# Kernel tuning notes

Hardware: AMD Instinct MI355X
Metric: run time of the kernel (lower is better)

Reference implementation:

```python
import jax, jax.numpy as jnp
import numpy as np


def setup_inputs() -> dict:
    key = jax.random.key(0)
    kq, kk, kv = jax.random.split(key, 3)
    B, H, N, D = 2, 16, 2048, 64
    q = jax.random.normal(kq, (B, H, N, D), dtype=jnp.float32)
    k = jax.random.normal(kk, (B, H, N, D), dtype=jnp.float32)
    v = jax.random.normal(kv, (B, H, N, D), dtype=jnp.float32)
    return {"q": q, "k": k, "v": v}


def reference(q, k, v):
    # RBF-kernel causal attention: logits = -relu(||q-k||^2) / sqrt(D)
    B, H, N, D = q.shape
    sm_scale = 1.0 / jnp.sqrt(jnp.asarray(D, dtype=q.dtype))
    q_sq = jnp.sum(q * q, axis=-1)              # [B,H,N]
    k_sq = jnp.sum(k * k, axis=-1)              # [B,H,N]
    qk = jnp.einsum("bhmd,bhnd->bhmn", q, k)    # [B,H,N,N]
    dist_sq = q_sq[..., :, None] + k_sq[..., None, :] - 2.0 * qk
    dist_sq = jnp.maximum(dist_sq, 0.0)         # relu on squared distance
    logits = -dist_sq * sm_scale
    # causal mask: query m attends to keys n <= m
    causal = jnp.tril(jnp.ones((N, N), dtype=bool))
    logits = jnp.where(causal, logits, -jnp.inf)
    p = jax.nn.softmax(logits, axis=-1)
    out = jnp.einsum("bhmn,bhnd->bhmd", p, v)
    return out
```

## Files before the change

### kernel.cpp

```cpp
#include <hip/hip_runtime.h>

#define NN 2048
#define DD 64
#define C1 0.36067376f
#define C1H 0.18033688f

typedef _Float16 h8 __attribute__((ext_vector_type(8)));
typedef _Float16 h4 __attribute__((ext_vector_type(4)));
typedef float f32x16 __attribute__((ext_vector_type(16)));

union H8U4 { h8 v; unsigned u[4]; };

__global__ __launch_bounds__(64) void prep(const float* __restrict__ k,
                                           const float* __restrict__ v,
                                           _Float16* __restrict__ Ks,
                                           _Float16* __restrict__ Vs,
                                           float* __restrict__ hk) {
    __shared__ _Float16 T[32][72];
    const int jj = blockIdx.x, bh = blockIdx.y, lane = threadIdx.x;
    const int ln = lane & 31, lh = lane >> 5;
    const size_t ibase = (size_t)bh * NN * DD + (size_t)jj * 32 * DD;

    {
        const float* kr = k + ibase + (size_t)ln * DD;
        float s = 0.f;
#pragma unroll
        for (int c = 0; c < 4; ++c) {
            float4 a = *(const float4*)&kr[16 * c + 8 * lh];
            float4 b = *(const float4*)&kr[16 * c + 8 * lh + 4];
            h8 o = {(_Float16)a.x, (_Float16)a.y, (_Float16)a.z, (_Float16)a.w,
                    (_Float16)b.x, (_Float16)b.y, (_Float16)b.z, (_Float16)b.w};
            *(h8*)&Ks[((size_t)bh * 16384 + jj * 256 + c * 64 + lh * 32 + ln) * 8] = o;
            s += a.x*a.x + a.y*a.y + a.z*a.z + a.w*a.w
               + b.x*b.x + b.y*b.y + b.z*b.z + b.w*b.w;
        }
        s += __shfl_xor(s, 32);
        if (lh == 0) hk[bh * NN + jj * 32 + ln] = s * C1H;
    }

#pragma unroll
    for (int t = 0; t < 8; ++t) {
        int f = lane + 64 * t;
        int row = f >> 4, c4 = (f & 15) * 4;
        float4 a = *(const float4*)&v[ibase + (size_t)row * DD + c4];
        h4 hv = {(_Float16)a.x, (_Float16)a.y, (_Float16)a.z, (_Float16)a.w};
        *(h4*)&T[row][c4] = hv;
    }
    __syncthreads();
#pragma unroll
    for (int oc = 0; oc < 4; ++oc) {
        int o = oc >> 1, c = oc & 1;
        h8 r;
#pragma unroll
        for (int jx = 0; jx < 8; ++jx) r[jx] = T[16 * c + 8 * lh + jx][32 * o + ln];
        *(h8*)&Vs[((size_t)bh * 16384 + jj * 256 + o * 128 + c * 64 + lh * 32 + ln) * 8] = r;
    }
}

__global__ __launch_bounds__(128, 2) void rbf_attn(
    const float* __restrict__ q, const _Float16* __restrict__ Ks,
    const _Float16* __restrict__ Vs, const float* __restrict__ hk,
    float* __restrict__ out)
{
    __shared__ float sm[64][34];
    const int tid = threadIdx.x;
    const int bh = blockIdx.x;
    const int qt = 63 - (int)blockIdx.y;
    const int wv = tid >> 6, lane = tid & 63;
    const int ln = lane & 31, lh = lane >> 5;
    const int qrow = qt * 32 + ln;
    const size_t fbase = (size_t)bh * NN * DD;

    h8 qf[4];
    {
        const float* qr = q + fbase + (size_t)qrow * DD;
#pragma unroll
        for (int c = 0; c < 4; ++c) {
            float4 a = *(const float4*)&qr[16 * c + 8 * lh];
            float4 b = *(const float4*)&qr[16 * c + 8 * lh + 4];
            qf[c] = h8{(_Float16)a.x, (_Float16)a.y, (_Float16)a.z, (_Float16)a.w,
                       (_Float16)b.x, (_Float16)b.y, (_Float16)b.z, (_Float16)b.w};
        }
    }

    const _Float16* Ksb = Ks + (size_t)bh * 131072;
    const _Float16* Vsb = Vs + (size_t)bh * 131072;
    const float4* hk4 = (const float4*)(hk + bh * NN);
    const int klq = (lh * 32 + ln) * 8;

    f32x16 O0, O1;
#pragma unroll
    for (int r = 0; r < 16; ++r) { O0[r] = 0.f; O1[r] = 0.f; }
    float lsum = 0.f, mrun = -INFINITY;

    const int T = qt + 1;
    const int half = (T + 1) >> 1;
    const int j0 = wv ? half : 0;
    const int j1 = wv ? T : half;

    auto loadT = [&](int jj, h8 (&kf)[4], h8 (&vf)[4], float4 (&hr)[4]) {
        const _Float16* kp = Ksb + (size_t)jj * 2048 + klq;
        const _Float16* vp = Vsb + (size_t)jj * 2048 + klq;
#pragma unroll
        for (int c = 0; c < 4; ++c) kf[c] = *(const h8*)(kp + c * 512);
#pragma unroll
        for (int oc = 0; oc < 4; ++oc)
            vf[oc] = *(const h8*)(vp + (oc >> 1) * 1024 + (oc & 1) * 512);
#pragma unroll
        for (int g = 0; g < 4; ++g) hr[g] = hk4[jj * 8 + g * 2 + lh];
    };

    auto comp = [&](int jj, h8 (&kf)[4], h8 (&vf)[4], float4 (&hr)[4]) {
        f32x16 S;
#pragma unroll
        for (int r = 0; r < 16; ++r) S[r] = 0.f;
#pragma unroll
        for (int c = 0; c < 4; ++c)
            S = __builtin_amdgcn_mfma_f32_32x32x16_f16(kf[c], qf[c], S, 0, 0, 0);

        const bool diag = (jj == qt);
        float x[16];
#pragma unroll
        for (int r = 0; r < 16; ++r) {
            const float* hf = (const float*)&hr[r >> 2];
            float xv = fmaf(S[r], C1, -hf[r & 3]);
            if (diag) {
                int keyloc = (r & 3) + 8 * (r >> 2) + 4 * lh;
                if (keyloc > ln) xv = -INFINITY;
            }
            x[r] = xv;
        }
        float mt = x[0];
#pragma unroll
        for (int r = 1; r < 16; ++r) mt = fmaxf(mt, x[r]);
        mt = fmaxf(mt, __shfl_xor(mt, 32));
        float mnew = fmaxf(mrun, mt);
        float alpha = __builtin_amdgcn_exp2f(mrun - mnew);
        mrun = mnew;
        float p[16], ps = 0.f;
#pragma unroll
        for (int r = 0; r < 16; ++r) {
            p[r] = __builtin_amdgcn_exp2f(x[r] - mnew);
            ps += p[r];
        }
        lsum = fmaf(lsum, alpha, ps);
#pragma unroll
        for (int r = 0; r < 16; ++r) { O0[r] *= alpha; O1[r] *= alpha; }

        unsigned pk[8];
#pragma unroll
        for (int hh = 0; hh < 8; ++hh) {
            auto pr = __builtin_amdgcn_cvt_pkrtz(p[2 * hh], p[2 * hh + 1]);
            unsigned pu; __builtin_memcpy(&pu, &pr, 4);
            pk[hh] = pu;
        }
#pragma unroll
        for (int s = 0; s < 2; ++s) {
            unsigned send0 = lh ? pk[4 * s + 0] : pk[4 * s + 2];
            unsigned send1 = lh ? pk[4 * s + 1] : pk[4 * s + 3];
            unsigned r0 = (unsigned)__shfl_xor((int)send0, 32);
            unsigned r1 = (unsigned)__shfl_xor((int)send1, 32);
            H8U4 pb;
            pb.u[0] = lh ? r0 : pk[4 * s + 0];
            pb.u[1] = lh ? r1 : pk[4 * s + 1];
            pb.u[2] = lh ? pk[4 * s + 2] : r0;
            pb.u[3] = lh ? pk[4 * s + 3] : r1;
            O0 = __builtin_amdgcn_mfma_f32_32x32x16_f16(vf[s], pb.v, O0, 0, 0, 0);
            O1 = __builtin_amdgcn_mfma_f32_32x32x16_f16(vf[2 + s], pb.v, O1, 0, 0, 0);
        }
    };

    h8 kfA[4], vfA[4]; float4 hrA[4];
    h8 kfB[4], vfB[4]; float4 hrB[4];
    if (j0 < j1) {
        loadT(j0, kfA, vfA, hrA);
        int jj = j0;
        while (true) {
            if (jj + 1 < j1) loadT(jj + 1, kfB, vfB, hrB);
            comp(jj, kfA, vfA, hrA);
            if (++jj >= j1) break;
            if (jj + 1 < j1) loadT(jj + 1, kfA, vfA, hrA);
            comp(jj, kfB, vfB, hrB);
            if (++jj >= j1) break;
        }
    }

    if (wv) {
#pragma unroll
        for (int r = 0; r < 16; ++r) { sm[lane][r] = O0[r]; sm[lane][16 + r] = O1[r]; }
        sm[lane][32] = lsum + __shfl_xor(lsum, 32);
        sm[lane][33] = mrun;
    }
    __syncthreads();
    if (!wv) {
        float l0 = lsum + __shfl_xor(lsum, 32);
        float l1 = sm[lane][32];
        float m1 = sm[lane][33];
        float m = fmaxf(mrun, m1);
        float a0 = __builtin_amdgcn_exp2f(mrun - m);
        float a1 = __builtin_amdgcn_exp2f(m1 - m);
        float lt = l0 * a0 + l1 * a1;
        float inv = 1.f / lt;
        float s0 = a0 * inv, s1 = a1 * inv;
        size_t ro = fbase + (size_t)qrow * DD;
#pragma unroll
        for (int g = 0; g < 4; ++g) {
            float4 o0 = make_float4(O0[4 * g + 0] * s0 + sm[lane][4 * g + 0] * s1,
                                    O0[4 * g + 1] * s0 + sm[lane][4 * g + 1] * s1,
                                    O0[4 * g + 2] * s0 + sm[lane][4 * g + 2] * s1,
                                    O0[4 * g + 3] * s0 + sm[lane][4 * g + 3] * s1);
            *(float4*)&out[ro + 8 * g + 4 * lh] = o0;
            float4 o1 = make_float4(O1[4 * g + 0] * s0 + sm[lane][16 + 4 * g + 0] * s1,
                                    O1[4 * g + 1] * s0 + sm[lane][16 + 4 * g + 1] * s1,
                                    O1[4 * g + 2] * s0 + sm[lane][16 + 4 * g + 2] * s1,
                                    O1[4 * g + 3] * s0 + sm[lane][16 + 4 * g + 3] * s1);
            *(float4*)&out[ro + 32 + 8 * g + 4 * lh] = o1;
        }
    }
}

extern "C" void kernel_launch(void* const* d_in, const int* in_sizes, int n_in,
                              void* d_out, int out_size, void* d_ws, size_t ws_size,
                              hipStream_t stream) {
    (void)in_sizes; (void)n_in; (void)out_size; (void)ws_size;
    const float* q = (const float*)d_in[0];
    const float* k = (const float*)d_in[1];
    const float* v = (const float*)d_in[2];
    float* out = (float*)d_out;

    float* hk = (float*)d_ws;
    _Float16* Ks = (_Float16*)((char*)d_ws + 262144);
    _Float16* Vs = (_Float16*)((char*)d_ws + 262144 + 8388608);

    prep<<<dim3(64, 32), 64, 0, stream>>>(k, v, Ks, Vs, hk);
    rbf_attn<<<dim3(32, 64), 128, 0, stream>>>(q, Ks, Vs, hk, out);
}
```

Before: 130.4 us.

## Split key range across four waves and defer softmax max rescaling

Each block now uses four waves instead of two, each covering a quarter of the causal key tiles, and merges the four partial results through shared memory at the end. The online softmax skips the max update and the rescale of accumulators and row sum unless some lane's logit exceeds the running max by a threshold. The goal is more parallelism per query tile with shorter serial loops, and less exp and multiply work per tile. The costs are a larger merge step, more shared memory, higher register pressure under the new launch bounds, and a risk that values grow before a deferred rescale happens.

```diff
diff --git a/kernel.cpp b/kernel.cpp
--- a/kernel.cpp
+++ b/kernel.cpp
@@ -4,6 +4,7 @@
 #define DD 64
 #define C1 0.36067376f
 #define C1H 0.18033688f
+#define DEFER_THR 8.0f
 
 typedef _Float16 h8 __attribute__((ext_vector_type(8)));
 typedef _Float16 h4 __attribute__((ext_vector_type(4)));
@@ -57,12 +58,12 @@
     }
 }
 
-__global__ __launch_bounds__(128, 2) void rbf_attn(
+__global__ __launch_bounds__(256, 4) void rbf_attn(
     const float* __restrict__ q, const _Float16* __restrict__ Ks,
     const _Float16* __restrict__ Vs, const float* __restrict__ hk,
     float* __restrict__ out)
 {
-    __shared__ float sm[64][34];
+    __shared__ float sm[3][64][35];
     const int tid = threadIdx.x;
     const int bh = blockIdx.x;
     const int qt = 63 - (int)blockIdx.y;
@@ -94,9 +95,8 @@
     float lsum = 0.f, mrun = -INFINITY;
 
     const int T = qt + 1;
-    const int half = (T + 1) >> 1;
-    const int j0 = wv ? half : 0;
-    const int j1 = wv ? T : half;
+    const int j0 = (wv * T) >> 2;
+    const int j1 = ((wv + 1) * T) >> 2;
 
     auto loadT = [&](int jj, h8 (&kf)[4], h8 (&vf)[4], float4 (&hr)[4]) {
         const _Float16* kp = Ksb + (size_t)jj * 2048 + klq;
@@ -119,33 +119,59 @@
             S = __builtin_amdgcn_mfma_f32_32x32x16_f16(kf[c], qf[c], S, 0, 0, 0);
 
         const bool diag = (jj == qt);
-        float x[16];
+        float p[16];
 #pragma unroll
         for (int r = 0; r < 16; ++r) {
             const float* hf = (const float*)&hr[r >> 2];
-            float xv = fmaf(S[r], C1, -hf[r & 3]);
+            float t = fmaf(S[r], C1, -(hf[r & 3] + mrun));
             if (diag) {
                 int keyloc = (r & 3) + 8 * (r >> 2) + 4 * lh;
-                if (keyloc > ln) xv = -INFINITY;
+                if (keyloc > ln) t = -INFINITY;
             }
-            x[r] = xv;
-        }
-        float mt = x[0];
-#pragma unroll
-        for (int r = 1; r < 16; ++r) mt = fmaxf(mt, x[r]);
-        mt = fmaxf(mt, __shfl_xor(mt, 32));
-        float mnew = fmaxf(mrun, mt);
-        float alpha = __builtin_amdgcn_exp2f(mrun - mnew);
-        mrun = mnew;
-        float p[16], ps = 0.f;
-#pragma unroll
-        for (int r = 0; r < 16; ++r) {
-            p[r] = __builtin_amdgcn_exp2f(x[r] - mnew);
-            ps += p[r];
-        }
-        lsum = fmaf(lsum, alpha, ps);
-#pragma unroll
-        for (int r = 0; r < 16; ++r) { O0[r] *= alpha; O1[r] *= alpha; }
+            p[r] = t;
+        }
+        float a0 = fmaxf(p[0], p[1]),  a1 = fmaxf(p[2], p[3]);
+        float a2 = fmaxf(p[4], p[5]),  a3 = fmaxf(p[6], p[7]);
+        float a4 = fmaxf(p[8], p[9]),  a5 = fmaxf(p[10], p[11]);
+        float a6 = fmaxf(p[12], p[13]), a7 = fmaxf(p[14], p[15]);
+        float b0 = fmaxf(a0, a1), b1 = fmaxf(a2, a3);
+        float b2 = fmaxf(a4, a5), b3 = fmaxf(a6, a7);
+        float fm = fmaxf(fmaxf(b0, b1), fmaxf(b2, b3));
+
+        if (__any(fm > DEFER_THR)) {
+#pragma unroll
+            for (int r = 0; r < 16; ++r) {
+                const float* hf = (const float*)&hr[r >> 2];
+                float xv = fmaf(S[r], C1, -hf[r & 3]);
+                if (diag) {
+                    int keyloc = (r & 3) + 8 * (r >> 2) + 4 * lh;
+                    if (keyloc > ln) xv = -INFINITY;
+                }
+                S[r] = xv;
+            }
+            float c0 = fmaxf(fmaxf(S[0], S[1]), fmaxf(S[2], S[3]));
+            float c1 = fmaxf(fmaxf(S[4], S[5]), fmaxf(S[6], S[7]));
+            float c2 = fmaxf(fmaxf(S[8], S[9]), fmaxf(S[10], S[11]));
+            float c3 = fmaxf(fmaxf(S[12], S[13]), fmaxf(S[14], S[15]));
+            float mtl = fmaxf(fmaxf(c0, c1), fmaxf(c2, c3));
+            float mt = fmaxf(mtl, __shfl_xor(mtl, 32));
+            float mnew = fmaxf(mrun, mt);
+            float alpha = __builtin_amdgcn_exp2f(mrun - mnew);
+#pragma unroll
+            for (int r = 0; r < 16; ++r)
+                p[r] = __builtin_amdgcn_exp2f(S[r] - mnew);
+            lsum *= alpha;
+#pragma unroll
+            for (int r = 0; r < 16; ++r) { O0[r] *= alpha; O1[r] *= alpha; }
+            mrun = mnew;
+        } else {
+#pragma unroll
+            for (int r = 0; r < 16; ++r)
+                p[r] = __builtin_amdgcn_exp2f(p[r]);
+        }
+        float ps = (((p[0] + p[1]) + (p[2] + p[3])) + ((p[4] + p[5]) + (p[6] + p[7])))
+                 + (((p[8] + p[9]) + (p[10] + p[11])) + ((p[12] + p[13]) + (p[14] + p[15])));
+        lsum += ps;
 
         unsigned pk[8];
 #pragma unroll
@@ -187,33 +213,42 @@
 
     if (wv) {
 #pragma unroll
-        for (int r = 0; r < 16; ++r) { sm[lane][r] = O0[r]; sm[lane][16 + r] = O1[r]; }
-        sm[lane][32] = lsum + __shfl_xor(lsum, 32);
-        sm[lane][33] = mrun;
+        for (int r = 0; r < 16; ++r) {
+            sm[wv - 1][lane][r] = O0[r];
+            sm[wv - 1][lane][16 + r] = O1[r];
+        }
+        sm[wv - 1][lane][32] = lsum + __shfl_xor(lsum, 32);
+        sm[wv - 1][lane][33] = mrun;
     }
     __syncthreads();
     if (!wv) {
         float l0 = lsum + __shfl_xor(lsum, 32);
-        float l1 = sm[lane][32];
-        float m1 = sm[lane][33];
-        float m = fmaxf(mrun, m1);
-        float a0 = __builtin_amdgcn_exp2f(mrun - m);
-        float a1 = __builtin_amdgcn_exp2f(m1 - m);
-        float lt = l0 * a0 + l1 * a1;
+        float m0 = mrun;
+        float m1 = sm[0][lane][33], m2 = sm[1][lane][33], m3 = sm[2][lane][33];
+        float m = fmaxf(fmaxf(m0, m1), fmaxf(m2, m3));
+        float w0 = __builtin_amdgcn_exp2f(m0 - m);
+        float w1 = __builtin_amdgcn_exp2f(m1 - m);
+        float w2 = __builtin_amdgcn_exp2f(m2 - m);
+        float w3 = __builtin_amdgcn_exp2f(m3 - m);
+        float lt = l0 * w0 + sm[0][lane][32] * w1 + sm[1][lane][32] * w2
+                 + sm[2][lane][32] * w3;
         float inv = 1.f / lt;
-        float s0 = a0 * inv, s1 = a1 * inv;
+        float s0 = w0 * inv, s1 = w1 * inv, s2 = w2 * inv, s3 = w3 * inv;
         size_t ro = fbase + (size_t)qrow * DD;
 #pragma unroll
         for (int g = 0; g < 4; ++g) {
-            float4 o0 = make_float4(O0[4 * g + 0] * s0 + sm[lane][4 * g + 0] * s1,
-                                    O0[4 * g + 1] * s0 + sm[lane][4 * g + 1] * s1,
-                                    O0[4 * g + 2] * s0 + sm[lane][4 * g + 2] * s1,
-                                    O0[4 * g + 3] * s0 + sm[lane][4 * g + 3] * s1);
+            float4 o0, o1;
+#pragma unroll
+            for (int e = 0; e < 4; ++e) {
+                int r = 4 * g + e;
+                float v0 = O0[r] * s0 + sm[0][lane][r] * s1
+                         + sm[1][lane][r] * s2 + sm[2][lane][r] * s3;
+                float v1 = O1[r] * s0 + sm[0][lane][16 + r] * s1
+                         + sm[1][lane][16 + r] * s2 + sm[2][lane][16 + r] * s3;
+                (&o0.x)[e] = v0;
+                (&o1.x)[e] = v1;
+            }
             *(float4*)&out[ro + 8 * g + 4 * lh] = o0;
-            float4 o1 = make_float4(O1[4 * g + 0] * s0 + sm[lane][16 + 4 * g + 0] * s1,
-                                    O1[4 * g + 1] * s0 + sm[lane][16 + 4 * g + 1] * s1,
-                                    O1[4 * g + 2] * s0 + sm[lane][16 + 4 * g + 2] * s1,
-                                    O1[4 * g + 3] * s0 + sm[lane][16 + 4 * g + 3] * s1);
             *(float4*)&out[ro + 32 + 8 * g + 4 * lh] = o1;
         }
     }
@@ -233,5 +268,5 @@
     _Float16* Vs = (_Float16*)((char*)d_ws + 262144 + 8388608);
 
     prep<<<dim3(64, 32), 64, 0, stream>>>(k, v, Ks, Vs, hk);
-    rbf_attn<<<dim3(32, 64), 128, 0, stream>>>(q, Ks, Vs, hk, out);
+    rbf_attn<<<dim3(32, 64), 256, 0, stream>>>(q, Ks, Vs, hk, out);
 }
```

Result: slower. 387.7 us (+197.3%).

## Defer softmax rescaling, prefetch only K, raise occupancy and add MFMA priority

Applied to the files above, without the earlier changes.

Adds a lazy online-softmax rescale. The running max is only updated, and O and lsum only rescaled, when some wave's logits exceed the stale max by a threshold, which removes most per-tile alpha multiplies and exp calls. Only K fragments are double-buffered now, while V and hk are loaded inside the compute step. This cuts register pressure so launch bounds can ask for 3 blocks per CU. s_setprio is wrapped around the MFMA sections to favour matrix issue. The risks are exposed V load latency and possible fp16 overflow of exp2 values up to 2^8 when rescaling is deferred.

```diff
diff --git a/kernel.cpp b/kernel.cpp
--- a/kernel.cpp
+++ b/kernel.cpp
@@ -4,6 +4,7 @@
 #define DD 64
 #define C1 0.36067376f
 #define C1H 0.18033688f
+#define DEFER_THR 8.0f
 
 typedef _Float16 h8 __attribute__((ext_vector_type(8)));
 typedef _Float16 h4 __attribute__((ext_vector_type(4)));
@@ -57,7 +58,7 @@
     }
 }
 
-__global__ __launch_bounds__(128, 2) void rbf_attn(
+__global__ __launch_bounds__(128, 3) void rbf_attn(
     const float* __restrict__ q, const _Float16* __restrict__ Ks,
     const _Float16* __restrict__ Vs, const float* __restrict__ hk,
     float* __restrict__ out)
@@ -98,62 +99,90 @@
     const int j0 = wv ? half : 0;
     const int j1 = wv ? T : half;
 
-    auto loadT = [&](int jj, h8 (&kf)[4], h8 (&vf)[4], float4 (&hr)[4]) {
+    auto loadK = [&](int jj, h8 (&kf)[4]) {
         const _Float16* kp = Ksb + (size_t)jj * 2048 + klq;
+#pragma unroll
+        for (int c = 0; c < 4; ++c) kf[c] = *(const h8*)(kp + c * 512);
+    };
+
+    auto comp = [&](int jj, h8 (&kf)[4]) {
+        float4 hr[4];
+#pragma unroll
+        for (int g = 0; g < 4; ++g) hr[g] = hk4[jj * 8 + g * 2 + lh];
+        h8 vf[4];
         const _Float16* vp = Vsb + (size_t)jj * 2048 + klq;
-#pragma unroll
-        for (int c = 0; c < 4; ++c) kf[c] = *(const h8*)(kp + c * 512);
 #pragma unroll
         for (int oc = 0; oc < 4; ++oc)
             vf[oc] = *(const h8*)(vp + (oc >> 1) * 1024 + (oc & 1) * 512);
-#pragma unroll
-        for (int g = 0; g < 4; ++g) hr[g] = hk4[jj * 8 + g * 2 + lh];
-    };
-
-    auto comp = [&](int jj, h8 (&kf)[4], h8 (&vf)[4], float4 (&hr)[4]) {
+
         f32x16 S;
 #pragma unroll
         for (int r = 0; r < 16; ++r) S[r] = 0.f;
+        __builtin_amdgcn_s_setprio(1);
 #pragma unroll
         for (int c = 0; c < 4; ++c)
             S = __builtin_amdgcn_mfma_f32_32x32x16_f16(kf[c], qf[c], S, 0, 0, 0);
+        __builtin_amdgcn_s_setprio(0);
 
         const bool diag = (jj == qt);
-        float x[16];
+        float t[16];
 #pragma unroll
         for (int r = 0; r < 16; ++r) {
             const float* hf = (const float*)&hr[r >> 2];
-            float xv = fmaf(S[r], C1, -hf[r & 3]);
+            float tv = fmaf(S[r], C1, -(hf[r & 3] + mrun));
             if (diag) {
                 int keyloc = (r & 3) + 8 * (r >> 2) + 4 * lh;
-                if (keyloc > ln) xv = -INFINITY;
+                if (keyloc > ln) tv = -INFINITY;
             }
-            x[r] = xv;
-        }
-        float mt = x[0];
-#pragma unroll
-        for (int r = 1; r < 16; ++r) mt = fmaxf(mt, x[r]);
-        mt = fmaxf(mt, __shfl_xor(mt, 32));
-        float mnew = fmaxf(mrun, mt);
-        float alpha = __builtin_amdgcn_exp2f(mrun - mnew);
-        mrun = mnew;
-        float p[16], ps = 0.f;
-#pragma unroll
-        for (int r = 0; r < 16; ++r) {
-            p[r] = __builtin_amdgcn_exp2f(x[r] - mnew);
-            ps += p[r];
-        }
-        lsum = fmaf(lsum, alpha, ps);
-#pragma unroll
-        for (int r = 0; r < 16; ++r) { O0[r] *= alpha; O1[r] *= alpha; }
+            t[r] = tv;
+        }
+        float a0 = fmaxf(t[0], t[1]),  a1 = fmaxf(t[2], t[3]);
+        float a2 = fmaxf(t[4], t[5]),  a3 = fmaxf(t[6], t[7]);
+        float a4 = fmaxf(t[8], t[9]),  a5 = fmaxf(t[10], t[11]);
+        float a6 = fmaxf(t[12], t[13]), a7 = fmaxf(t[14], t[15]);
+        float fm = fmaxf(fmaxf(fmaxf(a0, a1), fmaxf(a2, a3)),
+                         fmaxf(fmaxf(a4, a5), fmaxf(a6, a7)));
+
+        if (__any(fm > DEFER_THR)) {
+#pragma unroll
+            for (int r = 0; r < 16; ++r) {
+                const float* hf = (const float*)&hr[r >> 2];
+                float xv = fmaf(S[r], C1, -hf[r & 3]);
+                if (diag) {
+                    int keyloc = (r & 3) + 8 * (r >> 2) + 4 * lh;
+                    if (keyloc > ln) xv = -INFINITY;
+                }
+                S[r] = xv;
+            }
+            float c0 = fmaxf(fmaxf(S[0], S[1]), fmaxf(S[2], S[3]));
+            float c1 = fmaxf(fmaxf(S[4], S[5]), fmaxf(S[6], S[7]));
+            float c2 = fmaxf(fmaxf(S[8], S[9]), fmaxf(S[10], S[11]));
+            float c3 = fmaxf(fmaxf(S[12], S[13]), fmaxf(S[14], S[15]));
+            float mtl = fmaxf(fmaxf(c0, c1), fmaxf(c2, c3));
+            float mt = fmaxf(mtl, __shfl_xor(mtl, 32));
+            float mnew = fmaxf(mrun, mt);
+            float alpha = __builtin_amdgcn_exp2f(mrun - mnew);
+#pragma unroll
+            for (int r = 0; r < 16; ++r) t[r] = S[r] - mnew;
+            lsum *= alpha;
+#pragma unroll
+            for (int r = 0; r < 16; ++r) { O0[r] *= alpha; O1[r] *= alpha; }
+            mrun = mnew;
+        }
+#pragma unroll
+        for (int r = 0; r < 16; ++r) t[r] = __builtin_amdgcn_exp2f(t[r]);
+        float ps = (((t[0] + t[1]) + (t[2] + t[3])) + ((t[4] + t[5]) + (t[6] + t[7])))
+                 + (((t[8] + t[9]) + (t[10] + t[11])) + ((t[12] + t[13]) + (t[14] + t[15])));
+        lsum += ps;
 
         unsigned pk[8];
 #pragma unroll
         for (int hh = 0; hh < 8; ++hh) {
-            auto pr = __builtin_amdgcn_cvt_pkrtz(p[2 * hh], p[2 * hh + 1]);
+            auto pr = __builtin_amdgcn_cvt_pkrtz(t[2 * hh], t[2 * hh + 1]);
             unsigned pu; __builtin_memcpy(&pu, &pr, 4);
             pk[hh] = pu;
         }
+        __builtin_amdgcn_s_setprio(1);
 #pragma unroll
         for (int s = 0; s < 2; ++s) {
             unsigned send0 = lh ? pk[4 * s + 0] : pk[4 * s + 2];
@@ -168,19 +197,19 @@
             O0 = __builtin_amdgcn_mfma_f32_32x32x16_f16(vf[s], pb.v, O0, 0, 0, 0);
             O1 = __builtin_amdgcn_mfma_f32_32x32x16_f16(vf[2 + s], pb.v, O1, 0, 0, 0);
         }
+        __builtin_amdgcn_s_setprio(0);
     };
 
-    h8 kfA[4], vfA[4]; float4 hrA[4];
-    h8 kfB[4], vfB[4]; float4 hrB[4];
+    h8 kfA[4], kfB[4];
     if (j0 < j1) {
-        loadT(j0, kfA, vfA, hrA);
+        loadK(j0, kfA);
         int jj = j0;
         while (true) {
-            if (jj + 1 < j1) loadT(jj + 1, kfB, vfB, hrB);
-            comp(jj, kfA, vfA, hrA);
+            if (jj + 1 < j1) loadK(jj + 1, kfB);
+            comp(jj, kfA);
             if (++jj >= j1) break;
-            if (jj + 1 < j1) loadT(jj + 1, kfA, vfA, hrA);
-            comp(jj, kfB, vfB, hrB);
+            if (jj + 1 < j1) loadK(jj + 1, kfA);
+            comp(jj, kfB);
             if (++jj >= j1) break;
         }
     }
```

After: 164.1 us. +25.8%, slower.

## Software-pipeline QK MFMA ahead of softmax and use permlane32 swaps

Applied to the files above, without the earlier changes.

Restructures the main loop so the QK^T MFMA for the next key tile is issued before the softmax and PV of the current tile, with K fragments prefetched two tiles ahead. V and the key-norm loads move into the softmax/PV stage. Cross-half lane exchanges switch from __shfl_xor (ds_bpermute) to permlane32_swap, and the max and sum reductions become trees to shorten dependency chains. This overlaps matrix-core work with the exp/VALU work, at the cost of more live registers and V loads that are no longer prefetched.

```diff
diff --git a/kernel.cpp b/kernel.cpp
--- a/kernel.cpp
+++ b/kernel.cpp
@@ -10,6 +10,21 @@
 typedef float f32x16 __attribute__((ext_vector_type(16)));
 
 union H8U4 { h8 v; unsigned u[4]; };
+
+static __device__ inline float ph_max(float v) {
+    unsigned u; __builtin_memcpy(&u, &v, 4);
+    auto rr = __builtin_amdgcn_permlane32_swap(u, u, false, false);
+    unsigned r0 = rr[0], r1 = rr[1];
+    float a, b; __builtin_memcpy(&a, &r0, 4); __builtin_memcpy(&b, &r1, 4);
+    return fmaxf(a, b);
+}
+static __device__ inline float ph_sum(float v) {
+    unsigned u; __builtin_memcpy(&u, &v, 4);
+    auto rr = __builtin_amdgcn_permlane32_swap(u, u, false, false);
+    unsigned r0 = rr[0], r1 = rr[1];
+    float a, b; __builtin_memcpy(&a, &r0, 4); __builtin_memcpy(&b, &r1, 4);
+    return a + b;
+}
 
 __global__ __launch_bounds__(64) void prep(const float* __restrict__ k,
                                            const float* __restrict__ v,
@@ -98,25 +113,31 @@
     const int j0 = wv ? half : 0;
     const int j1 = wv ? T : half;
 
-    auto loadT = [&](int jj, h8 (&kf)[4], h8 (&vf)[4], float4 (&hr)[4]) {
+    auto loadK = [&](int jj, h8 (&kf)[4]) {
         const _Float16* kp = Ksb + (size_t)jj * 2048 + klq;
+#pragma unroll
+        for (int c = 0; c < 4; ++c) kf[c] = *(const h8*)(kp + c * 512);
+    };
+
+    auto qk = [&](const h8 (&kf)[4]) {
+        f32x16 S;
+#pragma unroll
+        for (int r = 0; r < 16; ++r) S[r] = 0.f;
+#pragma unroll
+        for (int c = 0; c < 4; ++c)
+            S = __builtin_amdgcn_mfma_f32_32x32x16_f16(kf[c], qf[c], S, 0, 0, 0);
+        return S;
+    };
+
+    auto smpv = [&](int jj, const f32x16& S) {
+        float4 hr[4];
+#pragma unroll
+        for (int g = 0; g < 4; ++g) hr[g] = hk4[jj * 8 + g * 2 + lh];
+        h8 vf[4];
         const _Float16* vp = Vsb + (size_t)jj * 2048 + klq;
-#pragma unroll
-        for (int c = 0; c < 4; ++c) kf[c] = *(const h8*)(kp + c * 512);
 #pragma unroll
         for (int oc = 0; oc < 4; ++oc)
             vf[oc] = *(const h8*)(vp + (oc >> 1) * 1024 + (oc & 1) * 512);
-#pragma unroll
-        for (int g = 0; g < 4; ++g) hr[g] = hk4[jj * 8 + g * 2 + lh];
-    };
-
-    auto comp = [&](int jj, h8 (&kf)[4], h8 (&vf)[4], float4 (&hr)[4]) {
-        f32x16 S;
-#pragma unroll
-        for (int r = 0; r < 16; ++r) S[r] = 0.f;
-#pragma unroll
-        for (int c = 0; c < 4; ++c)
-            S = __builtin_amdgcn_mfma_f32_32x32x16_f16(kf[c], qf[c], S, 0, 0, 0);
 
         const bool diag = (jj == qt);
         float x[16];
@@ -130,19 +151,21 @@
             }
             x[r] = xv;
         }
-        float mt = x[0];
-#pragma unroll
-        for (int r = 1; r < 16; ++r) mt = fmaxf(mt, x[r]);
-        mt = fmaxf(mt, __shfl_xor(mt, 32));
+        float a0 = fmaxf(x[0], x[1]),  a1 = fmaxf(x[2], x[3]);
+        float a2 = fmaxf(x[4], x[5]),  a3 = fmaxf(x[6], x[7]);
+        float a4 = fmaxf(x[8], x[9]),  a5 = fmaxf(x[10], x[11]);
+        float a6 = fmaxf(x[12], x[13]), a7 = fmaxf(x[14], x[15]);
+        float mt = fmaxf(fmaxf(fmaxf(a0, a1), fmaxf(a2, a3)),
+                         fmaxf(fmaxf(a4, a5), fmaxf(a6, a7)));
+        mt = ph_max(mt);
         float mnew = fmaxf(mrun, mt);
         float alpha = __builtin_amdgcn_exp2f(mrun - mnew);
         mrun = mnew;
-        float p[16], ps = 0.f;
-#pragma unroll
-        for (int r = 0; r < 16; ++r) {
-            p[r] = __builtin_amdgcn_exp2f(x[r] - mnew);
-            ps += p[r];
-        }
+        float p[16], ps;
+#pragma unroll
+        for (int r = 0; r < 16; ++r) p[r] = __builtin_amdgcn_exp2f(x[r] - mnew);
+        ps = (((p[0] + p[1]) + (p[2] + p[3])) + ((p[4] + p[5]) + (p[6] + p[7])))
+           + (((p[8] + p[9]) + (p[10] + p[11])) + ((p[12] + p[13]) + (p[14] + p[15])));
         lsum = fmaf(lsum, alpha, ps);
 #pragma unroll
         for (int r = 0; r < 16; ++r) { O0[r] *= alpha; O1[r] *= alpha; }
@@ -150,37 +173,42 @@
         unsigned pk[8];
 #pragma unroll
         for (int hh = 0; hh < 8; ++hh) {
-            auto pr = __builtin_amdgcn_cvt_pkrtz(p[2 * hh], p[2 * hh + 1]);
-            unsigned pu; __builtin_memcpy(&pu, &pr, 4);
+            auto prr = __builtin_amdgcn_cvt_pkrtz(p[2 * hh], p[2 * hh + 1]);
+            unsigned pu; __builtin_memcpy(&pu, &prr, 4);
             pk[hh] = pu;
         }
 #pragma unroll
         for (int s = 0; s < 2; ++s) {
-            unsigned send0 = lh ? pk[4 * s + 0] : pk[4 * s + 2];
-            unsigned send1 = lh ? pk[4 * s + 1] : pk[4 * s + 3];
-            unsigned r0 = (unsigned)__shfl_xor((int)send0, 32);
-            unsigned r1 = (unsigned)__shfl_xor((int)send1, 32);
+            auto r02 = __builtin_amdgcn_permlane32_swap(pk[4 * s + 0], pk[4 * s + 2],
+                                                        false, false);
+            auto r13 = __builtin_amdgcn_permlane32_swap(pk[4 * s + 1], pk[4 * s + 3],
+                                                        false, false);
             H8U4 pb;
-            pb.u[0] = lh ? r0 : pk[4 * s + 0];
-            pb.u[1] = lh ? r1 : pk[4 * s + 1];
-            pb.u[2] = lh ? pk[4 * s + 2] : r0;
-            pb.u[3] = lh ? pk[4 * s + 3] : r1;
+            pb.u[0] = r02[0];
+            pb.u[1] = r13[0];
+            pb.u[2] = r02[1];
+            pb.u[3] = r13[1];
             O0 = __builtin_amdgcn_mfma_f32_32x32x16_f16(vf[s], pb.v, O0, 0, 0, 0);
             O1 = __builtin_amdgcn_mfma_f32_32x32x16_f16(vf[2 + s], pb.v, O1, 0, 0, 0);
         }
     };
 
-    h8 kfA[4], vfA[4]; float4 hrA[4];
-    h8 kfB[4], vfB[4]; float4 hrB[4];
     if (j0 < j1) {
-        loadT(j0, kfA, vfA, hrA);
+        h8 kfA[4], kfB[4];
+        loadK(j0, kfA);
+        int jp = (j0 + 1 < j1) ? j0 + 1 : j1 - 1;
+        loadK(jp, kfB);
+        f32x16 Sa = qk(kfA);
+        f32x16 Sb;
         int jj = j0;
         while (true) {
-            if (jj + 1 < j1) loadT(jj + 1, kfB, vfB, hrB);
-            comp(jj, kfA, vfA, hrA);
+            Sb = qk(kfB);
+            { int jn = (jj + 2 < j1) ? jj + 2 : j1 - 1; loadK(jn, kfA); }
+            smpv(jj, Sa);
             if (++jj >= j1) break;
-            if (jj + 1 < j1) loadT(jj + 1, kfA, vfA, hrA);
-            comp(jj, kfB, vfB, hrB);
+            Sa = qk(kfA);
+            { int jn = (jj + 2 < j1) ? jj + 2 : j1 - 1; loadK(jn, kfB); }
+            smpv(jj, Sb);
             if (++jj >= j1) break;
         }
     }
@@ -188,12 +216,12 @@
     if (wv) {
 #pragma unroll
         for (int r = 0; r < 16; ++r) { sm[lane][r] = O0[r]; sm[lane][16 + r] = O1[r]; }
-        sm[lane][32] = lsum + __shfl_xor(lsum, 32);
+        sm[lane][32] = ph_sum(lsum);
         sm[lane][33] = mrun;
     }
     __syncthreads();
     if (!wv) {
-        float l0 = lsum + __shfl_xor(lsum, 32);
+        float l0 = ph_sum(lsum);
         float l1 = sm[lane][32];
         float m1 = sm[lane][33];
         float m = fmaxf(mrun, m1);
```

New measurement: 128.9 us. Within noise of the previous version (-1.1%).
